# Optimization experiments

Measured on AMD Instinct MI355X. Metric: run time of the kernel, lower is better.

## Reference

```python
import jax, jax.numpy as jnp
import numpy as np

D_MODEL = 192
D_STATE = 16
D_CONV = 3
D_INNER = 384  # expand * d_model
DT_RANK = 12   # ceil(d_model / 16)
BATCH = 8
SEQLEN = 4096


def setup_inputs() -> dict:
    key = jax.random.key(0)
    ks = jax.random.split(key, 8)
    s = 0.02
    dt_init_std = DT_RANK ** (-0.5)
    return {
        "hidden_states": jax.random.normal(ks[0], (BATCH, SEQLEN, D_MODEL), jnp.float32),
        "in_proj_w": jax.random.normal(ks[1], (2 * D_INNER, D_MODEL), jnp.float32) * s,
        "conv_w": jax.random.normal(ks[2], (D_INNER, 1, D_CONV), jnp.float32) * 0.1,
        "conv_b": jnp.zeros((D_INNER,), jnp.float32),
        "x_proj_w": jax.random.normal(ks[3], (DT_RANK + 2 * D_STATE, D_INNER), jnp.float32) * s,
        "dt_proj_w": jax.random.uniform(ks[4], (D_INNER, DT_RANK), jnp.float32, -dt_init_std, dt_init_std),
        "dt_proj_b": jax.random.uniform(ks[5], (D_INNER,), jnp.float32, -5.0, -2.0),
        "A_log": jnp.tile(jnp.log(jnp.arange(1, D_STATE + 1, dtype=jnp.float32))[None, :], (D_INNER, 1)),
        "D_skip": jnp.ones((D_INNER,), jnp.float32),
        "out_proj_w": jax.random.normal(ks[6], (D_MODEL, D_INNER), jnp.float32) * s,
    }


def reference(hidden_states, in_proj_w, conv_w, conv_b, x_proj_w,
              dt_proj_w, dt_proj_b, A_log, D_skip, out_proj_w):
    # in_proj: [B,L,d_model] -> [B,L,2*d_inner]
    xz = jnp.einsum('bld,ed->ble', hidden_states, in_proj_w)
    x, z = jnp.split(xz, 2, axis=-1)
    # depthwise conv1d over sequence, 'same' padding for kernel 3
    xc = jnp.transpose(x, (0, 2, 1))  # [B, d_inner, L]
    pad = (D_CONV - 1) // 2
    xc = jax.lax.conv_general_dilated(
        xc, conv_w, window_strides=(1,), padding=[(pad, pad)],
        feature_group_count=D_INNER, dimension_numbers=('NCH', 'OIH', 'NCH'))
    xc = xc + conv_b[None, :, None]
    x = jax.nn.silu(jnp.transpose(xc, (0, 2, 1)))  # [B, L, d_inner]
    # x_proj -> dt, B, C
    x_dbl = jnp.einsum('bld,ed->ble', x, x_proj_w)
    dt = x_dbl[..., :DT_RANK]
    Bm = x_dbl[..., DT_RANK:DT_RANK + D_STATE]
    Cm = x_dbl[..., DT_RANK + D_STATE:]
    dt = jnp.einsum('blr,dr->bld', dt, dt_proj_w) + dt_proj_b  # Linear adds bias
    dt = jax.nn.softplus(dt + dt_proj_b)  # original adds bias AGAIN inside scan (faithful)
    A = -jnp.exp(A_log)  # [d_inner, d_state]
    # selective scan over time (sequential recurrence -> lax.scan)
    xs = (jnp.swapaxes(dt, 0, 1), jnp.swapaxes(Bm, 0, 1),
          jnp.swapaxes(Cm, 0, 1), jnp.swapaxes(x, 0, 1))
    h0 = jnp.zeros((hidden_states.shape[0], D_INNER, D_STATE), x.dtype)

    def step(h, ts):
        dt_i, B_i, C_i, u_i = ts  # [B,d], [B,n], [B,n], [B,d]
        A_disc = jnp.exp(dt_i[:, :, None] * A[None])        # [B,d,n]
        h = A_disc * h + (dt_i * u_i)[:, :, None] * B_i[:, None, :]
        y = jnp.einsum('bdn,bn->bd', h, C_i) + D_skip * u_i
        return h, y

    _, ys = jax.lax.scan(step, h0, xs)  # ys: [L, B, d_inner]
    y = jnp.swapaxes(ys, 0, 1)
    y = y * jax.nn.silu(z)
    return jnp.einsum('bld,ed->ble', y, out_proj_w)
```

## Files before the change

kernel.cpp:

```cpp
#include <hip/hip_runtime.h>
#include <cmath>

#define BATCH 8
#define SEQLEN 4096
#define DMODEL 192
#define DINNER 384
#define DSTATE 16
#define DTRANK 12
#define XSTR 64
#define MTOT (BATCH*SEQLEN)
#define CH 32
#define NC (SEQLEN/CH)

typedef __bf16 bf16x8 __attribute__((ext_vector_type(8)));
typedef float f32x4 __attribute__((ext_vector_type(4)));
typedef unsigned short us8 __attribute__((ext_vector_type(8)));

__device__ __forceinline__ float silu_f(float x) { return x / (1.f + __expf(-x)); }
__device__ __forceinline__ unsigned short f2bf(float f) {
  unsigned u = __float_as_uint(f);
  return (unsigned short)((u + 0x7FFF + ((u >> 16) & 1)) >> 16);
}
__device__ __forceinline__ float bf2f(unsigned short b) {
  return __uint_as_float(((unsigned)b) << 16);
}

#define POW16(a, e1)                                                        \
  a[0] = (e1); a[1] = (e1) * (e1); a[2] = a[1] * (e1); a[3] = a[1] * a[1];  \
  a[4] = a[3] * (e1); a[5] = a[3] * a[1]; a[6] = a[3] * a[2];               \
  a[7] = a[3] * a[3]; a[8] = a[7] * (e1); a[9] = a[7] * a[1];               \
  a[10] = a[7] * a[2]; a[11] = a[7] * a[3]; a[12] = a[7] * a[4];            \
  a[13] = a[7] * a[5]; a[14] = a[7] * a[6]; a[15] = a[7] * a[7];

__global__ __launch_bounds__(256) void prep_k(const float* __restrict__ in_w,
                                              const float* __restrict__ xw,
                                              const float* __restrict__ ow,
                                              const float* __restrict__ dtw,
                                              unsigned short* __restrict__ wb,
                                              unsigned short* __restrict__ wxb,
                                              unsigned short* __restrict__ owb,
                                              float* __restrict__ dtwt) {
  const int i = blockIdx.x * 256 + threadIdx.x;
  if (i < 768 * DMODEL) wb[i] = f2bf(in_w[i]);
  if (i < XSTR * DINNER) wxb[i] = (i < 44 * DINNER) ? f2bf(xw[i]) : (unsigned short)0;
  if (i < DMODEL * DINNER) owb[i] = f2bf(ow[i]);
  if (i < DTRANK * DINNER) dtwt[i] = dtw[(i % DINNER) * DTRANK + (i / DINNER)];
}

__global__ __launch_bounds__(256) void gemm_in(const float* __restrict__ hs,
                                               const unsigned short* __restrict__ wb,
                                               unsigned short* __restrict__ xb,
                                               unsigned short* __restrict__ zb) {
  __shared__ unsigned short Als[128 * 40];
  __shared__ unsigned short Bls[128 * 40];
  const int tid = threadIdx.x;
  const int bid = blockIdx.y * 6 + blockIdx.x;
  const int lid = (bid & 7) * 192 + (bid >> 3);
  const int m0 = (lid / 6) * 128, n0 = (lid % 6) * 128;
  const int w = tid >> 6, l = tid & 63;
  const int wm = (w >> 1) * 64, wn = (w & 1) * 64;
  const int lr = l & 15, lk8 = (l >> 4) * 8;
  const int ar = tid >> 1, ag = (tid & 1) * 16;
  const float* Ap = hs + (size_t)(m0 + ar) * DMODEL + ag;
  const unsigned short* Wp = wb + (size_t)(n0 + ar) * DMODEL + ag;
  f32x4 acc[4][4];
#pragma unroll
  for (int i = 0; i < 4; i++)
#pragma unroll
    for (int j = 0; j < 4; j++) acc[i][j] = (f32x4){0.f, 0.f, 0.f, 0.f};
#pragma unroll
  for (int k0 = 0; k0 < DMODEL; k0 += 32) {
    float4 f0 = *(const float4*)(Ap + k0);
    float4 f1 = *(const float4*)(Ap + k0 + 4);
    float4 f2 = *(const float4*)(Ap + k0 + 8);
    float4 f3 = *(const float4*)(Ap + k0 + 12);
    us8 b0 = *(const us8*)(Wp + k0);
    us8 b1 = *(const us8*)(Wp + k0 + 8);
    us8 a0, a1;
    a0[0] = f2bf(f0.x); a0[1] = f2bf(f0.y); a0[2] = f2bf(f0.z); a0[3] = f2bf(f0.w);
    a0[4] = f2bf(f1.x); a0[5] = f2bf(f1.y); a0[6] = f2bf(f1.z); a0[7] = f2bf(f1.w);
    a1[0] = f2bf(f2.x); a1[1] = f2bf(f2.y); a1[2] = f2bf(f2.z); a1[3] = f2bf(f2.w);
    a1[4] = f2bf(f3.x); a1[5] = f2bf(f3.y); a1[6] = f2bf(f3.z); a1[7] = f2bf(f3.w);
    __syncthreads();
    *(us8*)(&Als[ar * 40 + ag]) = a0;
    *(us8*)(&Als[ar * 40 + ag + 8]) = a1;
    *(us8*)(&Bls[ar * 40 + ag]) = b0;
    *(us8*)(&Bls[ar * 40 + ag + 8]) = b1;
    __syncthreads();
    bf16x8 bfr[4];
#pragma unroll
    for (int fn = 0; fn < 4; fn++)
      bfr[fn] = *(const bf16x8*)(&Bls[(wn + fn * 16 + lr) * 40 + lk8]);
#pragma unroll
    for (int fm = 0; fm < 4; fm++) {
      bf16x8 af = *(const bf16x8*)(&Als[(wm + fm * 16 + lr) * 40 + lk8]);
#pragma unroll
      for (int fn = 0; fn < 4; fn++)
        acc[fm][fn] = __builtin_amdgcn_mfma_f32_16x16x32_bf16(af, bfr[fn], acc[fm][fn], 0, 0, 0);
    }
  }
  const int r0 = (l >> 4) * 4;
  unsigned short* dst = (n0 < DINNER) ? xb : zb;
  const int cb0 = (n0 < DINNER) ? n0 : (n0 - DINNER);
#pragma unroll
  for (int fm = 0; fm < 4; fm++) {
    const size_t rowb = (size_t)(m0 + wm + fm * 16 + r0);
#pragma unroll
    for (int fn = 0; fn < 4; fn++) {
      const int col = cb0 + wn + fn * 16 + lr;
#pragma unroll
      for (int r = 0; r < 4; r++)
        dst[(rowb + r) * DINNER + col] = f2bf(acc[fm][fn][r]);
    }
  }
}

__global__ __launch_bounds__(256) void conv_silu_k(const unsigned short* __restrict__ xb,
                                                   const float* __restrict__ cw,
                                                   const float* __restrict__ cb,
                                                   unsigned short* __restrict__ u16) {
  __shared__ float cws[DINNER * 4];
  const int tid = threadIdx.x;
  for (int i = tid; i < DINNER * 4; i += 256)
    cws[i] = (i < DINNER * 3) ? cw[i] : cb[i - DINNER * 3];
  __syncthreads();
  const int idx = blockIdx.x * 256 + tid;
  const int d = (idx % 48) * 8;
  const int m = idx / 48;
  const int l = m % SEQLEN;
  const us8 c0 = *(const us8*)(xb + (size_t)m * DINNER + d);
  const bool hm = (l > 0), hp = (l < SEQLEN - 1);
  us8 cm = c0, cp = c0;
  if (hm) cm = *(const us8*)(xb + (size_t)(m - 1) * DINNER + d);
  if (hp) cp = *(const us8*)(xb + (size_t)(m + 1) * DINNER + d);
  us8 o;
#pragma unroll
  for (int j = 0; j < 8; j++) {
    const int dj = d + j;
    float s = cws[DINNER * 3 + dj] + cws[dj * 3 + 1] * bf2f(c0[j]);
    if (hm) s += cws[dj * 3 + 0] * bf2f(cm[j]);
    if (hp) s += cws[dj * 3 + 2] * bf2f(cp[j]);
    o[j] = f2bf(silu_f(s));
  }
  *(us8*)(u16 + (size_t)m * DINNER + d) = o;
}

__global__ __launch_bounds__(256) void xproj_mfma(const unsigned short* __restrict__ u16,
                                                  const unsigned short* __restrict__ wxb,
                                                  float* __restrict__ xdbl) {
  __shared__ unsigned short Als[64 * 40];
  __shared__ unsigned short Bls[64 * 40];
  const int tid = threadIdx.x;
  const int m0 = blockIdx.x * 64;
  const int w = tid >> 6, l = tid & 63;
  const int wm = (w >> 1) * 32, wn = (w & 1) * 32;
  const int lr = l & 15, lk8 = (l >> 4) * 8;
  const int ar = tid >> 2, ag = (tid & 3) * 8;
  const unsigned short* Ap = u16 + (size_t)(m0 + ar) * DINNER + ag;
  const unsigned short* Wp = wxb + (size_t)ar * DINNER + ag;
  f32x4 acc[2][2];
#pragma unroll
  for (int i = 0; i < 2; i++)
#pragma unroll
    for (int j = 0; j < 2; j++) acc[i][j] = (f32x4){0.f, 0.f, 0.f, 0.f};
#pragma unroll
  for (int k0 = 0; k0 < DINNER; k0 += 32) {
    us8 a0 = *(const us8*)(Ap + k0);
    us8 b0 = *(const us8*)(Wp + k0);
    __syncthreads();
    *(us8*)(&Als[ar * 40 + ag]) = a0;
    *(us8*)(&Bls[ar * 40 + ag]) = b0;
    __syncthreads();
    bf16x8 bf0 = *(const bf16x8*)(&Bls[(wn + lr) * 40 + lk8]);
    bf16x8 bf1 = *(const bf16x8*)(&Bls[(wn + 16 + lr) * 40 + lk8]);
#pragma unroll
    for (int fm = 0; fm < 2; fm++) {
      bf16x8 af = *(const bf16x8*)(&Als[(wm + fm * 16 + lr) * 40 + lk8]);
      acc[fm][0] = __builtin_amdgcn_mfma_f32_16x16x32_bf16(af, bf0, acc[fm][0], 0, 0, 0);
      acc[fm][1] = __builtin_amdgcn_mfma_f32_16x16x32_bf16(af, bf1, acc[fm][1], 0, 0, 0);
    }
  }
  const int r0 = (l >> 4) * 4;
#pragma unroll
  for (int fm = 0; fm < 2; fm++) {
    const size_t rowb = (size_t)(m0 + wm + fm * 16 + r0);
#pragma unroll
    for (int fn = 0; fn < 2; fn++) {
      const int col = wn + fn * 16 + lr;
#pragma unroll
      for (int r = 0; r < 4; r++)
        xdbl[(rowb + r) * XSTR + col] = acc[fm][fn][r];
    }
  }
}

__global__ __launch_bounds__(256) void dtproj_k(const float* __restrict__ xdbl,
                                                const float* __restrict__ dtwt,
                                                const float* __restrict__ dtb,
                                                float* __restrict__ dt) {
  const int idx = blockIdx.x * 256 + threadIdx.x;
  const int q = (idx % 96) * 4;
  const size_t m = idx / 96;
  const float* xr = xdbl + m * XSTR;
  float xs[12];
  *(float4*)(xs) = *(const float4*)(xr);
  *(float4*)(xs + 4) = *(const float4*)(xr + 4);
  *(float4*)(xs + 8) = *(const float4*)(xr + 8);
  float4 bv = *(const float4*)(dtb + q);
  float4 s;
  s.x = 2.f * bv.x; s.y = 2.f * bv.y; s.z = 2.f * bv.z; s.w = 2.f * bv.w;
#pragma unroll
  for (int r = 0; r < DTRANK; r++) {
    float4 w4 = *(const float4*)(dtwt + r * DINNER + q);
    s.x = fmaf(xs[r], w4.x, s.x);
    s.y = fmaf(xs[r], w4.y, s.y);
    s.z = fmaf(xs[r], w4.z, s.z);
    s.w = fmaf(xs[r], w4.w, s.w);
  }
  float4 o;
  o.x = fmaxf(s.x, 0.f) + __logf(1.f + __expf(-fabsf(s.x)));
  o.y = fmaxf(s.y, 0.f) + __logf(1.f + __expf(-fabsf(s.y)));
  o.z = fmaxf(s.z, 0.f) + __logf(1.f + __expf(-fabsf(s.z)));
  o.w = fmaxf(s.w, 0.f) + __logf(1.f + __expf(-fabsf(s.w)));
  *(float4*)(dt + m * DINNER + q) = o;
}

__global__ __launch_bounds__(384, 6) void scan_part1(const float* __restrict__ dt,
                                                     const unsigned short* __restrict__ u16,
                                                     const float* __restrict__ xdbl,
                                                     const float* __restrict__ A_log,
                                                     float* __restrict__ Pbuf,
                                                     float* __restrict__ Sbuf) {
  __shared__ float Bs[CH][DSTATE];
  const int d = threadIdx.x;
  const int c = blockIdx.x, b = blockIdx.y;
  const size_t mbase = (size_t)b * SEQLEN + (size_t)c * CH;
  if (d < CH * 4) {
    const int r = d >> 2, q = d & 3;
    float4 v = *(const float4*)(xdbl + (mbase + r) * XSTR + DTRANK + q * 4);
    float* dst = &Bs[r][q * 4];
    dst[0] = v.x; dst[1] = v.y; dst[2] = v.z; dst[3] = v.w;
  }
  float Av[DSTATE];
#pragma unroll
  for (int q = 0; q < 4; q++) {
    float4 v = *(const float4*)(A_log + d * DSTATE + q * 4);
    Av[q * 4 + 0] = -__expf(v.x); Av[q * 4 + 1] = -__expf(v.y);
    Av[q * 4 + 2] = -__expf(v.z); Av[q * 4 + 3] = -__expf(v.w);
  }
  bool fastp = true;
#pragma unroll
  for (int n = 0; n < DSTATE; n++)
    fastp = fastp && (fabsf(Av[n] + (float)(n + 1)) < 1e-5f * (float)(n + 1));
  float h[DSTATE];
#pragma unroll
  for (int n = 0; n < DSTATE; n++) h[n] = 0.f;
  float dtsum = 0.f;
  __syncthreads();
  float dtv = dt[mbase * DINNER + d];
  float uv  = bf2f(u16[mbase * DINNER + d]);
  if (fastp) {
    for (int l = 0; l < CH; l++) {
      const int lp = (l + 1 < CH) ? (l + 1) : l;
      const float dtn = dt[(mbase + lp) * DINNER + d];
      const float un  = bf2f(u16[(mbase + lp) * DINNER + d]);
      const float du = dtv * uv;
      dtsum += dtv;
      float a[DSTATE];
      const float e1 = __expf(-dtv);
      POW16(a, e1)
#pragma unroll
      for (int n = 0; n < DSTATE; n++)
        h[n] = fmaf(a[n], h[n], du * Bs[l][n]);
      dtv = dtn; uv = un;
    }
  } else {
    for (int l = 0; l < CH; l++) {
      const int lp = (l + 1 < CH) ? (l + 1) : l;
      const float dtn = dt[(mbase + lp) * DINNER + d];
      const float un  = bf2f(u16[(mbase + lp) * DINNER + d]);
      const float du = dtv * uv;
      dtsum += dtv;
#pragma unroll
      for (int n = 0; n < DSTATE; n++) {
        const float a = __expf(dtv * Av[n]);
        h[n] = fmaf(a, h[n], du * Bs[l][n]);
      }
      dtv = dtn; uv = un;
    }
  }
  float P[DSTATE];
  if (fastp) {
    const float ep = __expf(-dtsum);
    POW16(P, ep)
  } else {
#pragma unroll
    for (int n = 0; n < DSTATE; n++) P[n] = __expf(dtsum * Av[n]);
  }
  float* Pp = Pbuf + ((size_t)(b * NC + c) * DINNER + d) * DSTATE;
  float* Sp = Sbuf + ((size_t)(b * NC + c) * DINNER + d) * DSTATE;
#pragma unroll
  for (int q = 0; q < 4; q++) {
    float4 pv, sv;
    pv.x = P[q * 4 + 0]; pv.y = P[q * 4 + 1]; pv.z = P[q * 4 + 2]; pv.w = P[q * 4 + 3];
    sv.x = h[q * 4 + 0]; sv.y = h[q * 4 + 1]; sv.z = h[q * 4 + 2]; sv.w = h[q * 4 + 3];
    *(float4*)(Pp + q * 4) = pv;
    *(float4*)(Sp + q * 4) = sv;
  }
}

__global__ __launch_bounds__(256) void scan_part2(float* __restrict__ Pbuf,
                                                  const float* __restrict__ Sbuf) {
  const int i = blockIdx.x * 256 + threadIdx.x;
  const int b = i / (DINNER * DSTATE);
  const int r = i % (DINNER * DSTATE);
  const size_t cs = DINNER * DSTATE;
  const size_t base = (size_t)b * NC * cs + r;
  float h = 0.f;
  for (int c0 = 0; c0 < NC; c0 += 8) {
    float pp[8], ss[8];
#pragma unroll
    for (int j = 0; j < 8; j++) {
      pp[j] = Pbuf[base + (size_t)(c0 + j) * cs];
      ss[j] = Sbuf[base + (size_t)(c0 + j) * cs];
    }
#pragma unroll
    for (int j = 0; j < 8; j++) {
      Pbuf[base + (size_t)(c0 + j) * cs] = h;
      h = fmaf(pp[j], h, ss[j]);
    }
  }
}

__global__ __launch_bounds__(384, 6) void scan_part3(const float* __restrict__ dt,
                                                     const unsigned short* __restrict__ u16,
                                                     const float* __restrict__ xdbl,
                                                     const float* __restrict__ A_log,
                                                     const float* __restrict__ Dsk,
                                                     const unsigned short* __restrict__ zb,
                                                     const float* __restrict__ H0,
                                                     unsigned short* __restrict__ yb) {
  __shared__ float BC[CH][2 * DSTATE];
  const int d = threadIdx.x;
  const int c = blockIdx.x, b = blockIdx.y;
  const size_t mbase = (size_t)b * SEQLEN + (size_t)c * CH;
  for (int i = d; i < CH * 8; i += 384) {
    const int r = i >> 3, q = i & 7;
    float4 v = *(const float4*)(xdbl + (mbase + r) * XSTR + DTRANK + q * 4);
    float* dst = &BC[r][q * 4];
    dst[0] = v.x; dst[1] = v.y; dst[2] = v.z; dst[3] = v.w;
  }
  float Av[DSTATE];
#pragma unroll
  for (int q = 0; q < 4; q++) {
    float4 v = *(const float4*)(A_log + d * DSTATE + q * 4);
    Av[q * 4 + 0] = -__expf(v.x); Av[q * 4 + 1] = -__expf(v.y);
    Av[q * 4 + 2] = -__expf(v.z); Av[q * 4 + 3] = -__expf(v.w);
  }
  bool fastp = true;
#pragma unroll
  for (int n = 0; n < DSTATE; n++)
    fastp = fastp && (fabsf(Av[n] + (float)(n + 1)) < 1e-5f * (float)(n + 1));
  const float Dv = Dsk[d];
  float h[DSTATE];
  {
    const float* Hp = H0 + ((size_t)(b * NC + c) * DINNER + d) * DSTATE;
#pragma unroll
    for (int q = 0; q < 4; q++) {
      float4 v = *(const float4*)(Hp + q * 4);
      h[q * 4 + 0] = v.x; h[q * 4 + 1] = v.y; h[q * 4 + 2] = v.z; h[q * 4 + 3] = v.w;
    }
  }
  __syncthreads();
  float dtv = dt[mbase * DINNER + d];
  float uv  = bf2f(u16[mbase * DINNER + d]);
  float zv  = bf2f(zb[mbase * DINNER + d]);
  if (fastp) {
    for (int l = 0; l < CH; l++) {
      const int lp = (l + 1 < CH) ? (l + 1) : l;
      const float dtn = dt[(mbase + lp) * DINNER + d];
      const float un  = bf2f(u16[(mbase + lp) * DINNER + d]);
      const float zn  = bf2f(zb[(mbase + lp) * DINNER + d]);
      const float du = dtv * uv;
      float yacc = Dv * uv;
      float a[DSTATE];
      const float e1 = __expf(-dtv);
      POW16(a, e1)
#pragma unroll
      for (int n = 0; n < DSTATE; n++) {
        h[n] = fmaf(a[n], h[n], du * BC[l][n]);
        yacc = fmaf(h[n], BC[l][DSTATE + n], yacc);
      }
      yb[(mbase + l) * DINNER + d] = f2bf(yacc * silu_f(zv));
      dtv = dtn; uv = un; zv = zn;
    }
  } else {
    for (int l = 0; l < CH; l++) {
      const int lp = (l + 1 < CH) ? (l + 1) : l;
      const float dtn = dt[(mbase + lp) * DINNER + d];
      const float un  = bf2f(u16[(mbase + lp) * DINNER + d]);
      const float zn  = bf2f(zb[(mbase + lp) * DINNER + d]);
      const float du = dtv * uv;
      float yacc = Dv * uv;
#pragma unroll
      for (int n = 0; n < DSTATE; n++) {
        const float a = __expf(dtv * Av[n]);
        h[n] = fmaf(a, h[n], du * BC[l][n]);
        yacc = fmaf(h[n], BC[l][DSTATE + n], yacc);
      }
      yb[(mbase + l) * DINNER + d] = f2bf(yacc * silu_f(zv));
      dtv = dtn; uv = un; zv = zn;
    }
  }
}

__global__ __launch_bounds__(256) void gemm_out(const unsigned short* __restrict__ yb,
                                                const unsigned short* __restrict__ owb,
                                                float* __restrict__ out) {
  __shared__ unsigned short Als[128 * 40];
  __shared__ unsigned short Bls[64 * 40];
  const int tid = threadIdx.x;
  const int bid = blockIdx.y * 3 + blockIdx.x;
  const int lid = (bid & 7) * 96 + (bid >> 3);
  const int m0 = (lid / 3) * 128, n0 = (lid % 3) * 64;
  const int w = tid >> 6, l = tid & 63;
  const int wm = (w >> 1) * 64, wn = (w & 1) * 32;
  const int lr = l & 15, lk8 = (l >> 4) * 8;
  const int ar = tid >> 1, ag = (tid & 1) * 16;
  const int br = tid >> 2, bg = (tid & 3) * 8;
  const unsigned short* Ap = yb + (size_t)(m0 + ar) * DINNER + ag;
  const unsigned short* Wp = owb + (size_t)(n0 + br) * DINNER + bg;
  f32x4 acc[4][2];
#pragma unroll
  for (int i = 0; i < 4; i++)
#pragma unroll
    for (int j = 0; j < 2; j++) acc[i][j] = (f32x4){0.f, 0.f, 0.f, 0.f};
#pragma unroll
  for (int k0 = 0; k0 < DINNER; k0 += 32) {
    us8 a0 = *(const us8*)(Ap + k0);
    us8 a1 = *(const us8*)(Ap + k0 + 8);
    us8 bv = *(const us8*)(Wp + k0);
    __syncthreads();
    *(us8*)(&Als[ar * 40 + ag]) = a0;
    *(us8*)(&Als[ar * 40 + ag + 8]) = a1;
    *(us8*)(&Bls[br * 40 + bg]) = bv;
    __syncthreads();
    bf16x8 b0 = *(const bf16x8*)(&Bls[(wn + lr) * 40 + lk8]);
    bf16x8 b1 = *(const bf16x8*)(&Bls[(wn + 16 + lr) * 40 + lk8]);
#pragma unroll
    for (int fm = 0; fm < 4; fm++) {
      bf16x8 af = *(const bf16x8*)(&Als[(wm + fm * 16 + lr) * 40 + lk8]);
      acc[fm][0] = __builtin_amdgcn_mfma_f32_16x16x32_bf16(af, b0, acc[fm][0], 0, 0, 0);
      acc[fm][1] = __builtin_amdgcn_mfma_f32_16x16x32_bf16(af, b1, acc[fm][1], 0, 0, 0);
    }
  }
  const int r0 = (l >> 4) * 4;
#pragma unroll
  for (int fm = 0; fm < 4; fm++) {
    const size_t rowb = (size_t)(m0 + wm + fm * 16 + r0);
#pragma unroll
    for (int fn = 0; fn < 2; fn++) {
      const int col = n0 + wn + fn * 16 + lr;
#pragma unroll
      for (int r = 0; r < 4; r++)
        out[(rowb + r) * DMODEL + col] = acc[fm][fn][r];
    }
  }
}

extern "C" void kernel_launch(void* const* d_in, const int* in_sizes, int n_in,
                              void* d_out, int out_size, void* d_ws, size_t ws_size,
                              hipStream_t stream) {
  const float* hs   = (const float*)d_in[0];
  const float* in_w = (const float*)d_in[1];
  const float* cw   = (const float*)d_in[2];
  const float* cb   = (const float*)d_in[3];
  const float* xw   = (const float*)d_in[4];
  const float* dtw  = (const float*)d_in[5];
  const float* dtb  = (const float*)d_in[6];
  const float* alog = (const float*)d_in[7];
  const float* dsk  = (const float*)d_in[8];
  const float* ow   = (const float*)d_in[9];
  float* out = (float*)d_out;

  char* ws = (char*)d_ws;
  unsigned short* xb  = (unsigned short*)(ws);
  unsigned short* u16 = (unsigned short*)(ws + 25165824);
  float* xdbl = (float*)(ws + 50331648);
  float* dt   = (float*)(ws + 58720256);
  float* Pbuf = (float*)(ws + 109051904);
  float* Sbuf = (float*)(ws + 134217728);
  unsigned short* zb  = (unsigned short*)(ws + 159383552);
  unsigned short* wb  = (unsigned short*)(ws + 184549376);
  unsigned short* wxb = (unsigned short*)(ws + 184844288);
  unsigned short* owb = (unsigned short*)(ws + 184893440);
  float* dtwt = (float*)(ws + 185040896);
  unsigned short* yb  = xb;

  prep_k<<<576, 256, 0, stream>>>(in_w, xw, ow, dtw, wb, wxb, owb, dtwt);
  gemm_in<<<dim3(6, 256), 256, 0, stream>>>(hs, wb, xb, zb);
  conv_silu_k<<<(MTOT * 48) / 256, 256, 0, stream>>>(xb, cw, cb, u16);
  xproj_mfma<<<MTOT / 64, 256, 0, stream>>>(u16, wxb, xdbl);
  dtproj_k<<<(MTOT * 96) / 256, 256, 0, stream>>>(xdbl, dtwt, dtb, dt);
  scan_part1<<<dim3(NC, BATCH), 384, 0, stream>>>(dt, u16, xdbl, alog, Pbuf, Sbuf);
  scan_part2<<<(BATCH * DINNER * DSTATE) / 256, 256, 0, stream>>>(Pbuf, Sbuf);
  scan_part3<<<dim3(NC, BATCH), 384, 0, stream>>>(dt, u16, xdbl, alog, dsk, zb, Pbuf, yb);
  gemm_out<<<dim3(3, 256), 256, 0, stream>>>(yb, owb, out);
}
```

Baseline: 200.2 us.

## Store dt in bf16 and pass chunk dt sums instead of decay products

```diff
diff --git a/kernel.cpp b/kernel.cpp
--- a/kernel.cpp
+++ b/kernel.cpp
@@ -197,7 +197,7 @@
 __global__ __launch_bounds__(256) void dtproj_k(const float* __restrict__ xdbl,
                                                 const float* __restrict__ dtwt,
                                                 const float* __restrict__ dtb,
-                                                float* __restrict__ dt) {
+                                                unsigned short* __restrict__ dt16) {
   const int idx = blockIdx.x * 256 + threadIdx.x;
   const int q = (idx % 96) * 4;
   const size_t m = idx / 96;
@@ -217,19 +217,19 @@
     s.z = fmaf(xs[r], w4.z, s.z);
     s.w = fmaf(xs[r], w4.w, s.w);
   }
-  float4 o;
-  o.x = fmaxf(s.x, 0.f) + __logf(1.f + __expf(-fabsf(s.x)));
-  o.y = fmaxf(s.y, 0.f) + __logf(1.f + __expf(-fabsf(s.y)));
-  o.z = fmaxf(s.z, 0.f) + __logf(1.f + __expf(-fabsf(s.z)));
-  o.w = fmaxf(s.w, 0.f) + __logf(1.f + __expf(-fabsf(s.w)));
-  *(float4*)(dt + m * DINNER + q) = o;
-}
-
-__global__ __launch_bounds__(384, 6) void scan_part1(const float* __restrict__ dt,
+  ushort4 o;
+  o.x = f2bf(fmaxf(s.x, 0.f) + __logf(1.f + __expf(-fabsf(s.x))));
+  o.y = f2bf(fmaxf(s.y, 0.f) + __logf(1.f + __expf(-fabsf(s.y))));
+  o.z = f2bf(fmaxf(s.z, 0.f) + __logf(1.f + __expf(-fabsf(s.z))));
+  o.w = f2bf(fmaxf(s.w, 0.f) + __logf(1.f + __expf(-fabsf(s.w))));
+  *(ushort4*)(dt16 + m * DINNER + q) = o;
+}
+
+__global__ __launch_bounds__(384, 6) void scan_part1(const unsigned short* __restrict__ dt16,
                                                      const unsigned short* __restrict__ u16,
                                                      const float* __restrict__ xdbl,
                                                      const float* __restrict__ A_log,
-                                                     float* __restrict__ Pbuf,
+                                                     float* __restrict__ Dsum,
                                                      float* __restrict__ Sbuf) {
   __shared__ float Bs[CH][DSTATE];
   const int d = threadIdx.x;
@@ -257,12 +257,12 @@
   for (int n = 0; n < DSTATE; n++) h[n] = 0.f;
   float dtsum = 0.f;
   __syncthreads();
-  float dtv = dt[mbase * DINNER + d];
+  float dtv = bf2f(dt16[mbase * DINNER + d]);
   float uv  = bf2f(u16[mbase * DINNER + d]);
   if (fastp) {
     for (int l = 0; l < CH; l++) {
       const int lp = (l + 1 < CH) ? (l + 1) : l;
-      const float dtn = dt[(mbase + lp) * DINNER + d];
+      const float dtn = bf2f(dt16[(mbase + lp) * DINNER + d]);
       const float un  = bf2f(u16[(mbase + lp) * DINNER + d]);
       const float du = dtv * uv;
       dtsum += dtv;
@@ -277,7 +277,7 @@
   } else {
     for (int l = 0; l < CH; l++) {
       const int lp = (l + 1 < CH) ? (l + 1) : l;
-      const float dtn = dt[(mbase + lp) * DINNER + d];
+      const float dtn = bf2f(dt16[(mbase + lp) * DINNER + d]);
       const float un  = bf2f(u16[(mbase + lp) * DINNER + d]);
       const float du = dtv * uv;
       dtsum += dtv;
@@ -289,50 +289,47 @@
       dtv = dtn; uv = un;
     }
   }
-  float P[DSTATE];
-  if (fastp) {
-    const float ep = __expf(-dtsum);
-    POW16(P, ep)
-  } else {
-#pragma unroll
-    for (int n = 0; n < DSTATE; n++) P[n] = __expf(dtsum * Av[n]);
-  }
-  float* Pp = Pbuf + ((size_t)(b * NC + c) * DINNER + d) * DSTATE;
+  Dsum[(size_t)(b * NC + c) * DINNER + d] = dtsum;
   float* Sp = Sbuf + ((size_t)(b * NC + c) * DINNER + d) * DSTATE;
 #pragma unroll
   for (int q = 0; q < 4; q++) {
-    float4 pv, sv;
-    pv.x = P[q * 4 + 0]; pv.y = P[q * 4 + 1]; pv.z = P[q * 4 + 2]; pv.w = P[q * 4 + 3];
+    float4 sv;
     sv.x = h[q * 4 + 0]; sv.y = h[q * 4 + 1]; sv.z = h[q * 4 + 2]; sv.w = h[q * 4 + 3];
-    *(float4*)(Pp + q * 4) = pv;
     *(float4*)(Sp + q * 4) = sv;
   }
 }
 
-__global__ __launch_bounds__(256) void scan_part2(float* __restrict__ Pbuf,
-                                                  const float* __restrict__ Sbuf) {
+__global__ __launch_bounds__(256) void scan_part2(const float* __restrict__ Dsum,
+                                                  const float* __restrict__ Sbuf,
+                                                  const float* __restrict__ A_log,
+                                                  float* __restrict__ Hbuf) {
   const int i = blockIdx.x * 256 + threadIdx.x;
   const int b = i / (DINNER * DSTATE);
   const int r = i % (DINNER * DSTATE);
+  const float Av = -__expf(A_log[r]);
   const size_t cs = DINNER * DSTATE;
-  const size_t base = (size_t)b * NC * cs + r;
+  const size_t sbase = (size_t)b * NC * cs + r;
+  const size_t dbase = (size_t)b * NC * DINNER + (r >> 4);
   float h = 0.f;
   for (int c0 = 0; c0 < NC; c0 += 8) {
-    float pp[8], ss[8];
+    float dd[8], ss[8];
 #pragma unroll
     for (int j = 0; j < 8; j++) {
-      pp[j] = Pbuf[base + (size_t)(c0 + j) * cs];
-      ss[j] = Sbuf[base + (size_t)(c0 + j) * cs];
-    }
+      dd[j] = Dsum[dbase + (size_t)(c0 + j) * DINNER];
+      ss[j] = Sbuf[sbase + (size_t)(c0 + j) * cs];
+    }
+    float pp[8];
+#pragma unroll
+    for (int j = 0; j < 8; j++) pp[j] = __expf(dd[j] * Av);
 #pragma unroll
     for (int j = 0; j < 8; j++) {
-      Pbuf[base + (size_t)(c0 + j) * cs] = h;
+      Hbuf[sbase + (size_t)(c0 + j) * cs] = h;
       h = fmaf(pp[j], h, ss[j]);
     }
   }
 }
 
-__global__ __launch_bounds__(384, 6) void scan_part3(const float* __restrict__ dt,
+__global__ __launch_bounds__(384, 6) void scan_part3(const unsigned short* __restrict__ dt16,
                                                      const unsigned short* __restrict__ u16,
                                                      const float* __restrict__ xdbl,
                                                      const float* __restrict__ A_log,
@@ -372,13 +369,13 @@
     }
   }
   __syncthreads();
-  float dtv = dt[mbase * DINNER + d];
+  float dtv = bf2f(dt16[mbase * DINNER + d]);
   float uv  = bf2f(u16[mbase * DINNER + d]);
   float zv  = bf2f(zb[mbase * DINNER + d]);
   if (fastp) {
     for (int l = 0; l < CH; l++) {
       const int lp = (l + 1 < CH) ? (l + 1) : l;
-      const float dtn = dt[(mbase + lp) * DINNER + d];
+      const float dtn = bf2f(dt16[(mbase + lp) * DINNER + d]);
       const float un  = bf2f(u16[(mbase + lp) * DINNER + d]);
       const float zn  = bf2f(zb[(mbase + lp) * DINNER + d]);
       const float du = dtv * uv;
@@ -397,7 +394,7 @@
   } else {
     for (int l = 0; l < CH; l++) {
       const int lp = (l + 1 < CH) ? (l + 1) : l;
-      const float dtn = dt[(mbase + lp) * DINNER + d];
+      const float dtn = bf2f(dt16[(mbase + lp) * DINNER + d]);
       const float un  = bf2f(u16[(mbase + lp) * DINNER + d]);
       const float zn  = bf2f(zb[(mbase + lp) * DINNER + d]);
       const float du = dtv * uv;
@@ -484,26 +481,27 @@
   float* out = (float*)d_out;
 
   char* ws = (char*)d_ws;
-  unsigned short* xb  = (unsigned short*)(ws);
-  unsigned short* u16 = (unsigned short*)(ws + 25165824);
+  unsigned short* xb   = (unsigned short*)(ws);
+  unsigned short* u16  = (unsigned short*)(ws + 25165824);
   float* xdbl = (float*)(ws + 50331648);
-  float* dt   = (float*)(ws + 58720256);
-  float* Pbuf = (float*)(ws + 109051904);
+  unsigned short* dt16 = (unsigned short*)(ws + 58720256);
+  float* Hbuf = (float*)(ws + 109051904);
   float* Sbuf = (float*)(ws + 134217728);
   unsigned short* zb  = (unsigned short*)(ws + 159383552);
   unsigned short* wb  = (unsigned short*)(ws + 184549376);
   unsigned short* wxb = (unsigned short*)(ws + 184844288);
   unsigned short* owb = (unsigned short*)(ws + 184893440);
   float* dtwt = (float*)(ws + 185040896);
+  float* Dsum = (float*)(ws + 185059328);
   unsigned short* yb  = xb;
 
   prep_k<<<576, 256, 0, stream>>>(in_w, xw, ow, dtw, wb, wxb, owb, dtwt);
   gemm_in<<<dim3(6, 256), 256, 0, stream>>>(hs, wb, xb, zb);
   conv_silu_k<<<(MTOT * 48) / 256, 256, 0, stream>>>(xb, cw, cb, u16);
   xproj_mfma<<<MTOT / 64, 256, 0, stream>>>(u16, wxb, xdbl);
-  dtproj_k<<<(MTOT * 96) / 256, 256, 0, stream>>>(xdbl, dtwt, dtb, dt);
-  scan_part1<<<dim3(NC, BATCH), 384, 0, stream>>>(dt, u16, xdbl, alog, Pbuf, Sbuf);
-  scan_part2<<<(BATCH * DINNER * DSTATE) / 256, 256, 0, stream>>>(Pbuf, Sbuf);
-  scan_part3<<<dim3(NC, BATCH), 384, 0, stream>>>(dt, u16, xdbl, alog, dsk, zb, Pbuf, yb);
+  dtproj_k<<<(MTOT * 96) / 256, 256, 0, stream>>>(xdbl, dtwt, dtb, dt16);
+  scan_part1<<<dim3(NC, BATCH), 384, 0, stream>>>(dt16, u16, xdbl, alog, Dsum, Sbuf);
+  scan_part2<<<(BATCH * DINNER * DSTATE) / 256, 256, 0, stream>>>(Dsum, Sbuf, alog, Hbuf);
+  scan_part3<<<dim3(NC, BATCH), 384, 0, stream>>>(dt16, u16, xdbl, alog, dsk, zb, Hbuf, yb);
   gemm_out<<<dim3(3, 256), 256, 0, stream>>>(yb, owb, out);
 }
```

Measured after the change: 183.9 us. 8.1% less time.
